# Performance work log

Hardware: AMD Instinct MI355X
Metric: run time of the kernel (lower is better)

## Reference

```python
import jax, jax.numpy as jnp
import numpy as np

N = 50000
E = 1600000
INPUT_DIM = 128
HEADS = 4
OUT_DIM = 32
LRELU_ALPHA = 0.2


def setup_inputs() -> dict:
    key = jax.random.key(0)
    k1, k2, k3, k4, k5 = jax.random.split(key, 5)
    gain = 1.0 / (1.0 + LRELU_ALPHA)
    input_proj = jax.random.normal(k1, (N, INPUT_DIM), dtype=jnp.float32)
    edge_index = jax.random.randint(k2, (2, E), 0, N, dtype=jnp.int64)
    W = jax.random.normal(k3, (INPUT_DIM, HEADS * OUT_DIM), dtype=jnp.float32) * (gain / INPUT_DIM) ** 0.5
    A_left = jax.random.normal(k4, (HEADS, OUT_DIM, 1), dtype=jnp.float32) * (gain / OUT_DIM)
    A_right = jax.random.normal(k5, (HEADS, OUT_DIM, 1), dtype=jnp.float32) * (gain / OUT_DIM)
    return {"input_proj": input_proj, "edge_index": edge_index, "W": W, "A_left": A_left, "A_right": A_right}


def reference(input_proj, edge_index, W, A_left, A_right):
    n = input_proj.shape[0]
    heads, out_dim = A_left.shape[0], A_left.shape[1]
    # Linear projection: [N, heads, out_dim]
    H = (input_proj @ W).reshape(n, heads, out_dim)
    # Per-node attention scores: [N, heads]
    H_s = jnp.einsum('nhd,hd->nh', H, A_left[..., 0])
    H_t = jnp.einsum('nhd,hd->nh', H, A_right[..., 0])
    src = edge_index[0]
    tgt = edge_index[1]
    # Edge scores: leaky_relu(H_s[src] + H_t[tgt]) -> [E, heads]
    e = H_s[src] + H_t[tgt]
    e = jnp.where(e > 0, e, LRELU_ALPHA * e)
    # Segment softmax over neighborhoods keyed by source node (global max shift, as in original)
    e = jnp.exp(e - jnp.max(e))
    denom = jax.ops.segment_sum(e, src, num_segments=n)  # [N, heads]
    alpha = e / (denom[src] + 1e-8)
    # Weighted scatter-add aggregation of target features: [N, heads, out_dim]
    msg = alpha[:, :, None] * H[tgt]
    agg = jax.ops.segment_sum(msg, src, num_segments=n)
    # concat_last=True -> [N, heads*out_dim], then ELU
    res = agg.reshape(n, heads * out_dim)
    return jax.nn.elu(res)
```

## Files before the change

### kernel.cpp

```cpp
#include <hip/hip_runtime.h>

#define DIM 128
#define HEADS 4
#define ODIM 32
#define LRELU 0.2f
#define PT 4096
#define CAP 9216

typedef unsigned int u32;
typedef unsigned short u16;
typedef unsigned char u8;

typedef __attribute__((ext_vector_type(8))) short bf16x8;
typedef __attribute__((ext_vector_type(4))) float f32x4;

__device__ __forceinline__ u16 f2bf(float f) {
    union { u32 u; float f; } x; x.f = f;
    u32 u = x.u;
    u32 r = u + 0x7FFFu + ((u >> 16) & 1u);
    return (u16)(r >> 16);
}
__device__ __forceinline__ float blo(u32 b) {
    union { u32 u; float f; } x; x.u = b << 16; return x.f;
}
__device__ __forceinline__ float bhi(u32 b) {
    union { u32 u; float f; } x; x.u = b & 0xFFFF0000u; return x.f;
}

__device__ __forceinline__ int scan256_excl(int v, int t, int* wsum) {
    int lane = t & 63, w = t >> 6;
    int inc = v;
    #pragma unroll
    for (int ofs = 1; ofs < 64; ofs <<= 1) {
        int x = __shfl_up(inc, ofs);
        if (lane >= ofs) inc += x;
    }
    __syncthreads();
    if (lane == 63) wsum[w] = inc;
    __syncthreads();
    int add = 0;
    #pragma unroll
    for (int j = 0; j < 4; ++j) add += (j < w) ? wsum[j] : 0;
    return inc - v + add;
}

__global__ __launch_bounds__(256) void prep_kernel(
    const float* __restrict__ W, u16* __restrict__ Wt, int* __restrict__ bcur)
{
    __shared__ u16 s[128 * 17];
    const int t = threadIdx.x;
    const int b = blockIdx.x;
    if (b == 0) bcur[t] = t * CAP;
    #pragma unroll
    for (int i = 0; i < 8; ++i) {
        int idx = i * 256 + t;
        int kk = idx >> 7;
        int nn = idx & 127;
        s[nn * 17 + kk] = f2bf(W[(b * 16 + kk) * 128 + nn]);
    }
    __syncthreads();
    #pragma unroll
    for (int i = 0; i < 8; ++i) {
        int idx = i * 256 + t;
        int nn = idx >> 4;
        int kk = idx & 15;
        Wt[nn * 128 + b * 16 + kk] = s[nn * 17 + kk];
    }
}

__device__ __forceinline__ void partition_body(
    char* smem, int bid, const int* __restrict__ ei, int* __restrict__ bcur,
    u32* __restrict__ part, int E, int n)
{
    u32* stage = (u32*)smem;
    u8*  sbkt  = (u8*)(smem + 16384);
    int (*lcnt4)[256] = (int (*)[256])(smem + 20480);
    int (*lcur4)[256] = (int (*)[256])(smem + 24576);
    int* loff  = (int*)(smem + 28672);
    int* ltot  = (int*)(smem + 29696);
    int* gbase = (int*)(smem + 30720);
    int* wsum  = (int*)(smem + 31744);
    const int t = threadIdx.x;
    const int wv = t >> 6;
    const int base = bid * PT;
    lcnt4[0][t] = 0; lcnt4[1][t] = 0; lcnt4[2][t] = 0; lcnt4[3][t] = 0;
    __syncthreads();

    int srcv[16], tgtv[16];
    #pragma unroll
    for (int i = 0; i < 16; ++i) {
        int e = base + i * 256 + t;
        srcv[i] = (e < E) ? ei[e] : -1;
    }
    #pragma unroll
    for (int i = 0; i < 16; ++i) {
        int e = base + i * 256 + t;
        tgtv[i] = (e < E) ? ei[E + e] : 0;
    }
    u32 key[16];
    int bkt[16];
    #pragma unroll
    for (int i = 0; i < 16; ++i) {
        bkt[i] = -1;
        key[i] = 0;
        if (srcv[i] >= 0) {
            int src = min(srcv[i], n - 1);
            int tgt = max(0, min(tgtv[i], n - 1));
            bkt[i] = src >> 8;
            key[i] = ((u32)(src & 255) << 17) | (u32)tgt;
        }
    }
    #pragma unroll
    for (int i = 0; i < 16; ++i)
        if (bkt[i] >= 0) atomicAdd(&lcnt4[wv][bkt[i]], 1);
    __syncthreads();
    int c0 = lcnt4[0][t], c1 = lcnt4[1][t], c2 = lcnt4[2][t], c3 = lcnt4[3][t];
    int total = c0 + c1 + c2 + c3;
    int ex = scan256_excl(total, t, wsum);
    loff[t] = ex;
    ltot[t] = total;
    lcur4[0][t] = ex;
    lcur4[1][t] = ex + c0;
    lcur4[2][t] = ex + c0 + c1;
    lcur4[3][t] = ex + c0 + c1 + c2;
    gbase[t] = (total > 0) ? atomicAdd(&bcur[t], total) : 0;
    __syncthreads();
    #pragma unroll
    for (int i = 0; i < 16; ++i) {
        if (bkt[i] >= 0) {
            int p = atomicAdd(&lcur4[wv][bkt[i]], 1);
            stage[p] = key[i];
            sbkt[p] = (u8)bkt[i];
        }
    }
    __syncthreads();
    int tot = loff[255] + ltot[255];
    for (int i = t; i < tot; i += 256) {
        int b = sbkt[i];
        int dst = gbase[b] + (i - loff[b]);
        if (dst < (b + 1) * CAP) part[dst] = stage[i];
    }
}

__device__ __forceinline__ void proj_body(
    char* smem, int bid, const float* __restrict__ X, const u16* __restrict__ Wt,
    const float* __restrict__ AL, const float* __restrict__ AR,
    u32* __restrict__ Hb, float* __restrict__ Hs, float* __restrict__ Ht, int n)
{
    float* sH  = (float*)smem;
    float* sAL = (float*)(smem + 33792);
    float* sAR = (float*)(smem + 34304);
    const int t = threadIdx.x;
    if (t < DIM) { sAL[t] = AL[t]; sAR[t] = AR[t]; }
    const int row0 = bid * 64;
    const int w = t >> 6, lane = t & 63;
    const int quad = lane >> 4, nIdx = lane & 15;
    const int m = row0 + w * 16 + nIdx;

    f32x4 acc[8];
    #pragma unroll
    for (int c = 0; c < 8; ++c) acc[c] = (f32x4){0.f, 0.f, 0.f, 0.f};

    #pragma unroll
    for (int kq = 0; kq < 4; ++kq) {
        union { bf16x8 v; u16 e[8]; } a;
        if (m < n) {
            const float* xp = &X[(size_t)m * DIM + kq * 32 + quad * 8];
            float4 x0 = *(const float4*)xp;
            float4 x1 = *(const float4*)(xp + 4);
            a.e[0] = f2bf(x0.x); a.e[1] = f2bf(x0.y);
            a.e[2] = f2bf(x0.z); a.e[3] = f2bf(x0.w);
            a.e[4] = f2bf(x1.x); a.e[5] = f2bf(x1.y);
            a.e[6] = f2bf(x1.z); a.e[7] = f2bf(x1.w);
        } else {
            #pragma unroll
            for (int j = 0; j < 8; ++j) a.e[j] = 0;
        }
        #pragma unroll
        for (int c = 0; c < 8; ++c) {
            bf16x8 b = *(const bf16x8*)&Wt[(c * 16 + nIdx) * DIM + kq * 32 + quad * 8];
            acc[c] = __builtin_amdgcn_mfma_f32_16x16x32_bf16(a.v, b, acc[c], 0, 0, 0);
        }
    }
    #pragma unroll
    for (int c = 0; c < 8; ++c)
        #pragma unroll
        for (int r = 0; r < 4; ++r)
            sH[(w * 16 + quad * 4 + r) * 132 + c * 16 + nIdx] = acc[c][r];
    __syncthreads();

    #pragma unroll
    for (int i = 0; i < 16; ++i) {
        int idx = i * 256 + t;
        int r = idx >> 6, d2 = idx & 63;
        int gr = row0 + r;
        if (gr < n) {
            float2 hv = *(const float2*)&sH[r * 132 + 2 * d2];
            Hb[(size_t)gr * 64 + d2] = ((u32)f2bf(hv.y) << 16) | (u32)f2bf(hv.x);
        }
    }
    {
        int r = t >> 2, h = t & 3;
        float s = 0.f, s2 = 0.f;
        #pragma unroll
        for (int q = 0; q < ODIM; q += 4) {
            float4 hv = *(const float4*)&sH[r * 132 + h * ODIM + q];
            s  += hv.x*sAL[h*ODIM+q] + hv.y*sAL[h*ODIM+q+1] + hv.z*sAL[h*ODIM+q+2] + hv.w*sAL[h*ODIM+q+3];
            s2 += hv.x*sAR[h*ODIM+q] + hv.y*sAR[h*ODIM+q+1] + hv.z*sAR[h*ODIM+q+2] + hv.w*sAR[h*ODIM+q+3];
        }
        int gr = row0 + r;
        if (gr < n) { Hs[gr * HEADS + h] = s; Ht[gr * HEADS + h] = s2; }
    }
}

__global__ __launch_bounds__(256) void fused_pp_kernel(
    const float* __restrict__ X, const u16* __restrict__ Wt,
    const float* __restrict__ AL, const float* __restrict__ AR,
    u32* __restrict__ Hb, float* __restrict__ Hs, float* __restrict__ Ht,
    const int* __restrict__ ei, int* __restrict__ bcur, u32* __restrict__ part,
    int n, int E, int partBlocks)
{
    __shared__ alignas(16) char smem[34816];
    if ((int)blockIdx.x < partBlocks)
        partition_body(smem, blockIdx.x, ei, bcur, part, E, n);
    else
        proj_body(smem, blockIdx.x - partBlocks, X, Wt, AL, AR, Hb, Hs, Ht, n);
}

__global__ __launch_bounds__(256) void csrfill_kernel(
    const u32* __restrict__ part, const int* __restrict__ bcur,
    int* __restrict__ off, int* __restrict__ csr_tgt, int n, int ntiles)
{
    __shared__ int lc4[4][128];
    __shared__ int lcur4[4][128];
    __shared__ int wsum[4];
    __shared__ int sBase, sCnt;
    const int blk = blockIdx.x, t = threadIdx.x;
    const int b = blk >> 1, half = blk & 1;
    const int wv = t >> 6;
    int myc = (t < ntiles) ? (bcur[t] - t * CAP) : 0;
    myc = max(0, min(myc, CAP));
    int ex = scan256_excl(myc, t, wsum);
    if (t == b) { sBase = ex; sCnt = myc; }
    if (t < 128) { lc4[0][t] = 0; lc4[1][t] = 0; lc4[2][t] = 0; lc4[3][t] = 0; }
    __syncthreads();
    const int pbase = b * CAP;
    const int base = sBase, cnt = sCnt;
    for (int i = t; i < cnt; i += 1024) {
        u32 k[4];
        #pragma unroll
        for (int u = 0; u < 4; ++u) {
            int idx = i + u * 256;
            k[u] = (idx < cnt) ? part[pbase + idx] : 0xFFFFFFFFu;
        }
        #pragma unroll
        for (int u = 0; u < 4; ++u) {
            int n8 = (int)(k[u] >> 17);
            if ((n8 >> 7) == half) atomicAdd(&lc4[wv][n8 & 127], 1);
        }
    }
    __syncthreads();
    int c0 = 0, c1 = 0, c2 = 0, c3 = 0, total = 0;
    if (t < 128) {
        c0 = lc4[0][t]; c1 = lc4[1][t]; c2 = lc4[2][t]; c3 = lc4[3][t];
        total = c0 + c1 + c2 + c3;
    }
    int ex2 = scan256_excl(total, t, wsum);
    int halfTot = wsum[0] + wsum[1];
    int myBase = base + (half ? (cnt - halfTot) : 0);
    if (t < 128) {
        lcur4[0][t] = ex2;
        lcur4[1][t] = ex2 + c0;
        lcur4[2][t] = ex2 + c0 + c1;
        lcur4[3][t] = ex2 + c0 + c1 + c2;
        int node = b * 256 + half * 128 + t;
        if (node < n) off[node] = myBase + ex2;
    }
    if (b == ntiles - 1 && half == 0 && t == 0) off[n] = base + cnt;
    __syncthreads();
    for (int i = t; i < cnt; i += 1024) {
        u32 k[4];
        #pragma unroll
        for (int u = 0; u < 4; ++u) {
            int idx = i + u * 256;
            k[u] = (idx < cnt) ? part[pbase + idx] : 0xFFFFFFFFu;
        }
        #pragma unroll
        for (int u = 0; u < 4; ++u) {
            int n8 = (int)(k[u] >> 17);
            if ((n8 >> 7) == half) {
                int p = atomicAdd(&lcur4[wv][n8 & 127], 1);
                csr_tgt[myBase + p] = (int)(k[u] & 0x1FFFFu);
            }
        }
    }
}

__global__ __launch_bounds__(256) void agg_kernel(
    const u32* __restrict__ Hb, const float* __restrict__ Hs,
    const float* __restrict__ Ht, const int* __restrict__ off,
    const int* __restrict__ csr_tgt, float2* __restrict__ out, int n, int E)
{
    int node = (blockIdx.x * 256 + threadIdx.x) >> 6;
    int L = threadIdx.x & 63;
    if (node >= n) return;
    int lo = off[node], hi = off[node + 1];
    lo = max(0, min(lo, E));
    hi = max(lo, min(hi, E));
    if (hi <= lo) {
        out[(size_t)node * 64 + L] = {0.f, 0.f};
        return;
    }
    const int h = L >> 4;
    const int jSel = L >> 2;
    const int hSel = L & 3;
    float4 hs4 = *(const float4*)&Hs[node * HEADS];
    float hsD = hSel == 0 ? hs4.x : hSel == 1 ? hs4.y : hSel == 2 ? hs4.z : hs4.w;
    float ax = 0.f, ay = 0.f, Sd = 0.f;

    for (int i = lo; i < hi; i += 32) {
        int tl = csr_tgt[min(i + (L & 31), hi - 1)];
        int tA = __shfl(tl, jSel);
        int tB = __shfl(tl, jSel + 16);
        float eA = hsD + Ht[tA * HEADS + hSel];
        float eB = hsD + Ht[tB * HEADS + hSel];
        float wA = (i + jSel < hi)
                       ? __expf(fminf(eA > 0.f ? eA : LRELU * eA, 30.f)) : 0.f;
        float wB = (i + jSel + 16 < hi)
                       ? __expf(fminf(eB > 0.f ? eB : LRELU * eB, 30.f)) : 0.f;
        Sd += wA + wB;
        u32 bb[32];
        #pragma unroll
        for (int j = 0; j < 32; ++j) {
            int sj = __builtin_amdgcn_readlane(tl, j);
            bb[j] = Hb[((size_t)(u32)sj << 6) + L];
        }
        #pragma unroll
        for (int j = 0; j < 16; ++j) {
            float wj = __shfl(wA, (j << 2) | h);
            ax += wj * blo(bb[j]);
            ay += wj * bhi(bb[j]);
        }
        #pragma unroll
        for (int j = 0; j < 16; ++j) {
            float wj = __shfl(wB, (j << 2) | h);
            ax += wj * blo(bb[j + 16]);
            ay += wj * bhi(bb[j + 16]);
        }
    }
    float S = 0.f;
    #pragma unroll
    for (int j = 0; j < 16; ++j) S += __shfl(Sd, (j << 2) | h);
    float inv = 1.f / (S + 1e-8f);
    float ox = ax * inv, oy = ay * inv;
    ox = ox > 0.f ? ox : (__expf(ox) - 1.f);
    oy = oy > 0.f ? oy : (__expf(oy) - 1.f);
    out[(size_t)node * 64 + L] = {ox, oy};
}

extern "C" void kernel_launch(void* const* d_in, const int* in_sizes, int n_in,
                              void* d_out, int out_size, void* d_ws, size_t ws_size,
                              hipStream_t stream) {
    const float* X  = (const float*)d_in[0];
    const int*   EI = (const int*)d_in[1];
    const float* W  = (const float*)d_in[2];
    const float* AL = (const float*)d_in[3];
    const float* AR = (const float*)d_in[4];
    const int n = in_sizes[0] / DIM;
    const int E = in_sizes[1] / 2;
    const int ntiles = (n + 255) / 256;

    char* ws = (char*)d_ws;
    size_t o = 0;
    auto alloc = [&](size_t bytes) -> void* {
        o = (o + 255) & ~(size_t)255;
        void* p = ws + o;
        o += bytes;
        return p;
    };
    int*   bcur    = (int*)alloc(256 * 4);
    u16*   Wt      = (u16*)alloc((size_t)DIM * DIM * 2);
    int*   off     = (int*)alloc((size_t)(n + 1) * 4);
    float* Hs      = (float*)alloc((size_t)n * HEADS * 4);
    float* Ht      = (float*)alloc((size_t)n * HEADS * 4);
    int*   csr_tgt = (int*)alloc((size_t)E * 4);
    u32*   part    = (u32*)alloc((size_t)ntiles * CAP * 4);
    u32*   Hb      = (u32*)alloc((size_t)n * 64 * 4);

    const int PB = (E + PT - 1) / PT;
    const int JB = (n + 63) / 64;

    prep_kernel<<<8, 256, 0, stream>>>(W, Wt, bcur);
    fused_pp_kernel<<<PB + JB, 256, 0, stream>>>(
        X, Wt, AL, AR, Hb, Hs, Ht, EI, bcur, part, n, E, PB);
    csrfill_kernel<<<ntiles * 2, 256, 0, stream>>>(part, bcur, off, csr_tgt, n, ntiles);
    agg_kernel<<<(n + 3) / 4, 256, 0, stream>>>(
        Hb, Hs, Ht, off, csr_tgt, (float2*)d_out, n, E);
}
```

Baseline: 185.6 us.

## Process eight nodes per wavefront in aggregation with prefetched offsets and targets

The aggregation kernel now assigns eight consecutive nodes to each wavefront instead of one. It loads all nine CSR offsets and the eight nodes' source scores with one lane-parallel read, then prefetches the first 32 target indices for every node before any aggregation starts. This hides the dependent-load latency of off and csr_tgt and cuts the number of waves launched, at the cost of more registers and fewer waves for load balancing across the GPU.

```diff
diff --git a/kernel.cpp b/kernel.cpp
--- a/kernel.cpp
+++ b/kernel.cpp
@@ -6,6 +6,7 @@
 #define LRELU 0.2f
 #define PT 4096
 #define CAP 9216
+#define NPW 8
 
 typedef unsigned int u32;
 typedef unsigned short u16;
@@ -301,61 +302,115 @@
     const float* __restrict__ Ht, const int* __restrict__ off,
     const int* __restrict__ csr_tgt, float2* __restrict__ out, int n, int E)
 {
-    int node = (blockIdx.x * 256 + threadIdx.x) >> 6;
-    int L = threadIdx.x & 63;
-    if (node >= n) return;
-    int lo = off[node], hi = off[node + 1];
-    lo = max(0, min(lo, E));
-    hi = max(lo, min(hi, E));
-    if (hi <= lo) {
-        out[(size_t)node * 64 + L] = {0.f, 0.f};
-        return;
-    }
+    const int wid = (blockIdx.x * 256 + threadIdx.x) >> 6;
+    const int L = threadIdx.x & 63;
+    const int n0 = wid * NPW;
+    if (n0 >= n) return;
+
     const int h = L >> 4;
     const int jSel = L >> 2;
     const int hSel = L & 3;
-    float4 hs4 = *(const float4*)&Hs[node * HEADS];
-    float hsD = hSel == 0 ? hs4.x : hSel == 1 ? hs4.y : hSel == 2 ? hs4.z : hs4.w;
-    float ax = 0.f, ay = 0.f, Sd = 0.f;
-
-    for (int i = lo; i < hi; i += 32) {
-        int tl = csr_tgt[min(i + (L & 31), hi - 1)];
-        int tA = __shfl(tl, jSel);
-        int tB = __shfl(tl, jSel + 16);
-        float eA = hsD + Ht[tA * HEADS + hSel];
-        float eB = hsD + Ht[tB * HEADS + hSel];
-        float wA = (i + jSel < hi)
-                       ? __expf(fminf(eA > 0.f ? eA : LRELU * eA, 30.f)) : 0.f;
-        float wB = (i + jSel + 16 < hi)
-                       ? __expf(fminf(eB > 0.f ? eB : LRELU * eB, 30.f)) : 0.f;
-        Sd += wA + wB;
-        u32 bb[32];
-        #pragma unroll
-        for (int j = 0; j < 32; ++j) {
-            int sj = __builtin_amdgcn_readlane(tl, j);
-            bb[j] = Hb[((size_t)(u32)sj << 6) + L];
-        }
-        #pragma unroll
-        for (int j = 0; j < 16; ++j) {
-            float wj = __shfl(wA, (j << 2) | h);
-            ax += wj * blo(bb[j]);
-            ay += wj * bhi(bb[j]);
-        }
-        #pragma unroll
-        for (int j = 0; j < 16; ++j) {
-            float wj = __shfl(wB, (j << 2) | h);
-            ax += wj * blo(bb[j + 16]);
-            ay += wj * bhi(bb[j + 16]);
-        }
-    }
-    float S = 0.f;
-    #pragma unroll
-    for (int j = 0; j < 16; ++j) S += __shfl(Sd, (j << 2) | h);
-    float inv = 1.f / (S + 1e-8f);
-    float ox = ax * inv, oy = ay * inv;
-    ox = ox > 0.f ? ox : (__expf(ox) - 1.f);
-    oy = oy > 0.f ? oy : (__expf(oy) - 1.f);
-    out[(size_t)node * 64 + L] = {ox, oy};
+
+    int offv = 0;
+    if (L <= NPW) offv = off[min(n0 + L, n)];
+    float hsv = 0.f;
+    {
+        int nd = n0 + (L >> 2);
+        if (L < NPW * HEADS && nd < n) hsv = Hs[nd * HEADS + (L & 3)];
+    }
+
+    int tlv[NPW];
+    #pragma unroll
+    for (int k = 0; k < NPW; ++k) {
+        int lo = __shfl(offv, k), hi = __shfl(offv, k + 1);
+        lo = max(0, min(lo, E)); hi = max(lo, min(hi, E));
+        tlv[k] = 0;
+        if (n0 + k < n && hi > lo)
+            tlv[k] = csr_tgt[min(lo + (L & 31), hi - 1)];
+    }
+
+    #pragma unroll
+    for (int k = 0; k < NPW; ++k) {
+        int node = n0 + k;
+        if (node < n) {
+            int lo = __shfl(offv, k), hi = __shfl(offv, k + 1);
+            lo = max(0, min(lo, E)); hi = max(lo, min(hi, E));
+            if (hi <= lo) {
+                out[(size_t)node * 64 + L] = {0.f, 0.f};
+            } else {
+                float hsD = __shfl(hsv, (k << 2) | hSel);
+                float ax = 0.f, ay = 0.f, Sd = 0.f;
+                {
+                    int tl = tlv[k];
+                    int tA = __shfl(tl, jSel);
+                    int tB = __shfl(tl, jSel + 16);
+                    float eA = hsD + Ht[tA * HEADS + hSel];
+                    float eB = hsD + Ht[tB * HEADS + hSel];
+                    float wA = (lo + jSel < hi)
+                        ? __expf(fminf(eA > 0.f ? eA : LRELU * eA, 30.f)) : 0.f;
+                    float wB = (lo + jSel + 16 < hi)
+                        ? __expf(fminf(eB > 0.f ? eB : LRELU * eB, 30.f)) : 0.f;
+                    Sd += wA + wB;
+                    u32 bb[32];
+                    #pragma unroll
+                    for (int j = 0; j < 32; ++j) {
+                        int sj = __builtin_amdgcn_readlane(tl, j);
+                        bb[j] = Hb[((size_t)(u32)sj << 6) + L];
+                    }
+                    #pragma unroll
+                    for (int j = 0; j < 16; ++j) {
+                        float wj = __shfl(wA, (j << 2) | h);
+                        ax += wj * blo(bb[j]);
+                        ay += wj * bhi(bb[j]);
+                    }
+                    #pragma unroll
+                    for (int j = 0; j < 16; ++j) {
+                        float wj = __shfl(wB, (j << 2) | h);
+                        ax += wj * blo(bb[j + 16]);
+                        ay += wj * bhi(bb[j + 16]);
+                    }
+                }
+                for (int i = lo + 32; i < hi; i += 32) {
+                    int tl = csr_tgt[min(i + (L & 31), hi - 1)];
+                    int tA = __shfl(tl, jSel);
+                    int tB = __shfl(tl, jSel + 16);
+                    float eA = hsD + Ht[tA * HEADS + hSel];
+                    float eB = hsD + Ht[tB * HEADS + hSel];
+                    float wA = (i + jSel < hi)
+                        ? __expf(fminf(eA > 0.f ? eA : LRELU * eA, 30.f)) : 0.f;
+                    float wB = (i + jSel + 16 < hi)
+                        ? __expf(fminf(eB > 0.f ? eB : LRELU * eB, 30.f)) : 0.f;
+                    Sd += wA + wB;
+                    u32 bb[32];
+                    #pragma unroll
+                    for (int j = 0; j < 32; ++j) {
+                        int sj = __builtin_amdgcn_readlane(tl, j);
+                        bb[j] = Hb[((size_t)(u32)sj << 6) + L];
+                    }
+                    #pragma unroll
+                    for (int j = 0; j < 16; ++j) {
+                        float wj = __shfl(wA, (j << 2) | h);
+                        ax += wj * blo(bb[j]);
+                        ay += wj * bhi(bb[j]);
+                    }
+                    #pragma unroll
+                    for (int j = 0; j < 16; ++j) {
+                        float wj = __shfl(wB, (j << 2) | h);
+                        ax += wj * blo(bb[j + 16]);
+                        ay += wj * bhi(bb[j + 16]);
+                    }
+                }
+                float S = 0.f;
+                #pragma unroll
+                for (int j = 0; j < 16; ++j) S += __shfl(Sd, (j << 2) | h);
+                float inv = 1.f / (S + 1e-8f);
+                float ox = ax * inv, oy = ay * inv;
+                ox = ox > 0.f ? ox : (__expf(ox) - 1.f);
+                oy = oy > 0.f ? oy : (__expf(oy) - 1.f);
+                out[(size_t)node * 64 + L] = {ox, oy};
+            }
+        }
+    }
 }
 
 extern "C" void kernel_launch(void* const* d_in, const int* in_sizes, int n_in,
@@ -394,6 +449,6 @@
     fused_pp_kernel<<<PB + JB, 256, 0, stream>>>(
         X, Wt, AL, AR, Hb, Hs, Ht, EI, bcur, part, n, E, PB);
     csrfill_kernel<<<ntiles * 2, 256, 0, stream>>>(part, bcur, off, csr_tgt, n, ntiles);
-    agg_kernel<<<(n + 3) / 4, 256, 0, stream>>>(
+    agg_kernel<<<(n + 4 * NPW - 1) / (4 * NPW), 256, 0, stream>>>(
         Hb, Hs, Ht, off, csr_tgt, (float2*)d_out, n, E);
 }
```

New measurement: 200.1 us. +7.8%, slower.
